# Optimization experiments

Hardware: AMD Instinct MI355X
Metric: run time of the kernel (lower is better)

Reference implementation:

```python
import jax, jax.numpy as jnp
import numpy as np

WINDOW = 128
CAUSAL = True
LOOK_BACKWARD = 1
LOOK_FORWARD = 0  # causal forces look_forward = 0


def _look_around(x, backward, forward, pad_value, dim):
    # pad along window axis (axis=1), then concat shifted slices along `dim`
    nw = x.shape[1]
    pad_cfg = [(0, 0)] * x.ndim
    pad_cfg[1] = (backward, forward)
    padded = jnp.pad(x, pad_cfg, constant_values=pad_value)
    slices = [padded[:, i:i + nw] for i in range(forward + backward + 1)]
    return jnp.concatenate(slices, axis=dim)


def setup_inputs() -> dict:
    key = jax.random.key(0)
    kq, kk, kv = jax.random.split(key, 3)
    shape = (2, 16, 4096, 64)
    return {
        "q": jax.random.normal(kq, shape, dtype=jnp.float32),
        "k": jax.random.normal(kk, shape, dtype=jnp.float32),
        "v": jax.random.normal(kv, shape, dtype=jnp.float32),
    }


def reference(q, k, v):
    b, h, t, e = q.shape
    scale = e ** (-0.5)
    windows = t // WINDOW  # t assumed divisible by WINDOW (pad_to_multiple is no-op)

    # merge batch and heads, bucket into windows
    bq = q.reshape(b * h, windows, WINDOW, e)
    bk = k.reshape(b * h, windows, WINDOW, e)
    bv = v.reshape(b * h, windows, WINDOW, e)

    # look-around gather of key/value windows: j-dim = WINDOW*(1+back+fwd)
    bk = _look_around(bk, LOOK_BACKWARD, LOOK_FORWARD, 0.0, dim=2)
    bv = _look_around(bv, LOOK_BACKWARD, LOOK_FORWARD, 0.0, dim=2)

    # positional indices for masking
    bq_t = jnp.arange(t).reshape(1, windows, WINDOW)
    bq_k = _look_around(bq_t, LOOK_BACKWARD, LOOK_FORWARD, -1, dim=2)

    mask = (bq_k == -1)[:, :, None, :]  # (1, w, 1, j) padded positions
    if CAUSAL:
        mask = mask | (bq_t[:, :, :, None] < bq_k[:, :, None, :])

    dots = jnp.einsum('bwie,bwje->bwij', bq * scale, bk)
    mask_value = -jnp.finfo(dots.dtype).max
    dots = jnp.where(mask, mask_value, dots)
    attn = jax.nn.softmax(dots.astype(jnp.float32), axis=-1).astype(dots.dtype)
    out = jnp.einsum('bwij,bwje->bwie', attn, bv)
    return out.reshape(b, h, t, e)
```

## Files before the change

### kernel.cpp

```cpp
#include <hip/hip_runtime.h>

#define T_DIM 4096
#define E_DIM 64
#define WIN   128
#define NWIN  (T_DIM / WIN)
#define VT_LD 264
#define PS_LD 36

typedef __bf16  bf16x8 __attribute__((ext_vector_type(8)));
typedef __bf16  bf16x4 __attribute__((ext_vector_type(4)));
typedef float   f32x16 __attribute__((ext_vector_type(16)));

__global__ __launch_bounds__(256, 2)
void la_fwd(const float* __restrict__ Q, const float* __restrict__ K,
            const float* __restrict__ V, float* __restrict__ O)
{
  __shared__ __bf16 Vt[E_DIM * VT_LD];
  __shared__ __bf16 Ps[4 * 32 * PS_LD];

  const int tid  = threadIdx.x;
  const int lane = tid & 63;
  const int wid  = tid >> 6;
  const int col  = lane & 31;
  const int half = lane >> 5;

  const int w  = blockIdx.x;
  const int bh = blockIdx.y;

  const float* Qb = Q + (size_t)bh * T_DIM * E_DIM;
  const float* Kb = K + (size_t)bh * T_DIM * E_DIM;
  const float* Vb = V + (size_t)bh * T_DIM * E_DIM;
  float*       Ob = O + (size_t)bh * T_DIM * E_DIM;

  const int q0 = w * WIN;
  const int k0 = (w - 1) * WIN;

  {
    const int j = tid;
    int jg = k0 + j; if (jg < 0) jg = 0;
    const float* vrow = Vb + (size_t)jg * E_DIM;
#pragma unroll
    for (int c4 = 0; c4 < 16; ++c4) {
      const float4 vv = *(const float4*)(vrow + c4 * 4);
      const int e = c4 * 4;
      Vt[(e + 0) * VT_LD + j] = (__bf16)vv.x;
      Vt[(e + 1) * VT_LD + j] = (__bf16)vv.y;
      Vt[(e + 2) * VT_LD + j] = (__bf16)vv.z;
      Vt[(e + 3) * VT_LD + j] = (__bf16)vv.w;
    }
  }

  const float QS = 0.125f * 1.44269504088896340736f;
  bf16x8 aq[4];
  {
    const float* qrow = Qb + (size_t)(q0 + wid * 32 + col) * E_DIM;
#pragma unroll
    for (int c = 0; c < 4; ++c) {
      const float* p = qrow + c * 16 + half * 8;
      const float4 x = *(const float4*)(p);
      const float4 y = *(const float4*)(p + 4);
      bf16x8 a;
      a[0] = (__bf16)(x.x * QS); a[1] = (__bf16)(x.y * QS);
      a[2] = (__bf16)(x.z * QS); a[3] = (__bf16)(x.w * QS);
      a[4] = (__bf16)(y.x * QS); a[5] = (__bf16)(y.y * QS);
      a[6] = (__bf16)(y.z * QS); a[7] = (__bf16)(y.w * QS);
      aq[c] = a;
    }
  }

  __syncthreads();

  f32x16 sacc[8];
#pragma unroll
  for (int kb = 0; kb < 8; ++kb)
#pragma unroll
    for (int r = 0; r < 16; ++r) sacc[kb][r] = 0.0f;

#pragma unroll
  for (int kb = 0; kb < 8; ++kb) {
    int jg = k0 + kb * 32 + col; if (jg < 0) jg = 0;
    const float* krow = Kb + (size_t)jg * E_DIM;
#pragma unroll
    for (int c = 0; c < 4; ++c) {
      const float* p = krow + c * 16 + half * 8;
      const float4 x = *(const float4*)(p);
      const float4 y = *(const float4*)(p + 4);
      bf16x8 b;
      b[0] = (__bf16)x.x; b[1] = (__bf16)x.y; b[2] = (__bf16)x.z; b[3] = (__bf16)x.w;
      b[4] = (__bf16)y.x; b[5] = (__bf16)y.y; b[6] = (__bf16)y.z; b[7] = (__bf16)y.w;
      sacc[kb] = __builtin_amdgcn_mfma_f32_32x32x16_bf16(aq[c], b, sacc[kb], 0, 0, 0);
    }
  }

  float rinv[16];
#pragma unroll
  for (int r = 0; r < 16; ++r) {
    const int row  = (r & 3) + 8 * (r >> 2) + 4 * half;
    const int iloc = wid * 32 + row;
    float m = -3.0e38f;
#pragma unroll
    for (int kb = 0; kb < 8; ++kb) {
      const int jloc = kb * 32 + col;
      const bool masked = (jloc > iloc + WIN) || (w == 0 && jloc < WIN);
      const float s = masked ? -3.0e38f : sacc[kb][r];
      sacc[kb][r] = s;
      m = fmaxf(m, s);
    }
#pragma unroll
    for (int d = 1; d <= 16; d <<= 1) m = fmaxf(m, __shfl_xor(m, d));
    float l = 0.0f;
#pragma unroll
    for (int kb = 0; kb < 8; ++kb) {
      const float p = __builtin_amdgcn_exp2f(sacc[kb][r] - m);
      sacc[kb][r] = p;
      l += p;
    }
#pragma unroll
    for (int d = 1; d <= 16; d <<= 1) l += __shfl_xor(l, d);
    rinv[r] = __builtin_amdgcn_rcpf(l);
  }

  f32x16 oacc[2];
#pragma unroll
  for (int et = 0; et < 2; ++et)
#pragma unroll
    for (int r = 0; r < 16; ++r) oacc[et][r] = 0.0f;

  __bf16* myPs = Ps + wid * (32 * PS_LD);
#pragma unroll
  for (int kb = 0; kb < 8; ++kb) {
#pragma unroll
    for (int r = 0; r < 16; ++r) {
      const int row = (r & 3) + 8 * (r >> 2) + 4 * half;
      myPs[row * PS_LD + col] = (__bf16)sacc[kb][r];
    }
    bf16x8 ap[2];
#pragma unroll
    for (int c2 = 0; c2 < 2; ++c2) {
      const __bf16* rp = myPs + col * PS_LD + c2 * 16 + half * 8;
      union { bf16x8 v8; bf16x4 v4[2]; } u;
      u.v4[0] = *(const bf16x4*)(rp);
      u.v4[1] = *(const bf16x4*)(rp + 4);
      ap[c2] = u.v8;
    }
#pragma unroll
    for (int c2 = 0; c2 < 2; ++c2) {
      const int j0 = kb * 32 + c2 * 16 + half * 8;
#pragma unroll
      for (int et = 0; et < 2; ++et) {
        const int e = et * 32 + col;
        const bf16x8 bv = *(const bf16x8*)(Vt + e * VT_LD + j0);
        oacc[et] = __builtin_amdgcn_mfma_f32_32x32x16_bf16(ap[c2], bv, oacc[et], 0, 0, 0);
      }
    }
  }

#pragma unroll
  for (int r = 0; r < 16; ++r) {
    const int row = (r & 3) + 8 * (r >> 2) + 4 * half;
    const int ig  = q0 + wid * 32 + row;
    float* op = Ob + (size_t)ig * E_DIM;
    op[col]      = oacc[0][r] * rinv[r];
    op[col + 32] = oacc[1][r] * rinv[r];
  }
}

extern "C" void kernel_launch(void* const* d_in, const int* in_sizes, int n_in,
                              void* d_out, int out_size, void* d_ws, size_t ws_size,
                              hipStream_t stream) {
  const float* Q = (const float*)d_in[0];
  const float* K = (const float*)d_in[1];
  const float* V = (const float*)d_in[2];
  float*       O = (float*)d_out;
  const int bh = in_sizes[0] / (T_DIM * E_DIM);
  dim3 grid(NWIN, bh);
  la_fwd<<<grid, 256, 0, stream>>>(Q, K, V, O);
}
```

Before: 160.2 us.

## Stream K/V windows through LDS with online softmax and skip masked tiles

Restructures the kernel into two stages, previous window then current window. Each stage stages K (bf16, row layout) and transposed V into LDS and runs an online-softmax flash-style loop over 32-key blocks. Fully masked blocks (future keys, and the previous window when w==0) are skipped, row reductions use DPP/swizzle instead of shfl, and occupancy is raised to 3 blocks per SM. This removes redundant masked MMA/exp work and the large score register array, at the cost of extra syncs and per-block rescaling.

```diff
diff --git a/kernel.cpp b/kernel.cpp
--- a/kernel.cpp
+++ b/kernel.cpp
@@ -4,19 +4,45 @@
 #define E_DIM 64
 #define WIN   128
 #define NWIN  (T_DIM / WIN)
-#define VT_LD 264
+#define KS_LD 72
+#define VT_LD 136
 #define PS_LD 36
 
 typedef __bf16  bf16x8 __attribute__((ext_vector_type(8)));
 typedef __bf16  bf16x4 __attribute__((ext_vector_type(4)));
 typedef float   f32x16 __attribute__((ext_vector_type(16)));
 
-__global__ __launch_bounds__(256, 2)
+template<int CTRL>
+__device__ __forceinline__ float dppf(float x) {
+  return __int_as_float(__builtin_amdgcn_update_dpp(0, __float_as_int(x), CTRL, 0xf, 0xf, false));
+}
+__device__ __forceinline__ float swz16(float x) {
+  return __int_as_float(__builtin_amdgcn_ds_swizzle(__float_as_int(x), 0x401F));
+}
+__device__ __forceinline__ float rmax32(float x) {
+  x = fmaxf(x, dppf<0xB1>(x));
+  x = fmaxf(x, dppf<0x4E>(x));
+  x = fmaxf(x, dppf<0x141>(x));
+  x = fmaxf(x, dppf<0x140>(x));
+  x = fmaxf(x, swz16(x));
+  return x;
+}
+__device__ __forceinline__ float rsum32(float x) {
+  x += dppf<0xB1>(x);
+  x += dppf<0x4E>(x);
+  x += dppf<0x141>(x);
+  x += dppf<0x140>(x);
+  x += swz16(x);
+  return x;
+}
+
+__global__ __launch_bounds__(256, 3)
 void la_fwd(const float* __restrict__ Q, const float* __restrict__ K,
             const float* __restrict__ V, float* __restrict__ O)
 {
+  __shared__ __bf16 Ks[WIN * KS_LD];
   __shared__ __bf16 Vt[E_DIM * VT_LD];
-  __shared__ __bf16 Ps[4 * 32 * PS_LD];
+  __shared__ __bf16 Psm[4 * 32 * PS_LD];
 
   const int tid  = threadIdx.x;
   const int lane = tid & 63;
@@ -33,22 +59,6 @@
   float*       Ob = O + (size_t)bh * T_DIM * E_DIM;
 
   const int q0 = w * WIN;
-  const int k0 = (w - 1) * WIN;
-
-  {
-    const int j = tid;
-    int jg = k0 + j; if (jg < 0) jg = 0;
-    const float* vrow = Vb + (size_t)jg * E_DIM;
-#pragma unroll
-    for (int c4 = 0; c4 < 16; ++c4) {
-      const float4 vv = *(const float4*)(vrow + c4 * 4);
-      const int e = c4 * 4;
-      Vt[(e + 0) * VT_LD + j] = (__bf16)vv.x;
-      Vt[(e + 1) * VT_LD + j] = (__bf16)vv.y;
-      Vt[(e + 2) * VT_LD + j] = (__bf16)vv.z;
-      Vt[(e + 3) * VT_LD + j] = (__bf16)vv.w;
-    }
-  }
 
   const float QS = 0.125f * 1.44269504088896340736f;
   bf16x8 aq[4];
@@ -60,84 +70,71 @@
       const float4 x = *(const float4*)(p);
       const float4 y = *(const float4*)(p + 4);
       bf16x8 a;
-      a[0] = (__bf16)(x.x * QS); a[1] = (__bf16)(x.y * QS);
-      a[2] = (__bf16)(x.z * QS); a[3] = (__bf16)(x.w * QS);
-      a[4] = (__bf16)(y.x * QS); a[5] = (__bf16)(y.y * QS);
-      a[6] = (__bf16)(y.z * QS); a[7] = (__bf16)(y.w * QS);
+      a[0]=(__bf16)(x.x*QS); a[1]=(__bf16)(x.y*QS); a[2]=(__bf16)(x.z*QS); a[3]=(__bf16)(x.w*QS);
+      a[4]=(__bf16)(y.x*QS); a[5]=(__bf16)(y.y*QS); a[6]=(__bf16)(y.z*QS); a[7]=(__bf16)(y.w*QS);
       aq[c] = a;
     }
   }
 
-  __syncthreads();
-
-  f32x16 sacc[8];
+  float mr[16], lr[16];
+  f32x16 oacc[2];
 #pragma unroll
-  for (int kb = 0; kb < 8; ++kb)
-#pragma unroll
-    for (int r = 0; r < 16; ++r) sacc[kb][r] = 0.0f;
-
-#pragma unroll
-  for (int kb = 0; kb < 8; ++kb) {
-    int jg = k0 + kb * 32 + col; if (jg < 0) jg = 0;
-    const float* krow = Kb + (size_t)jg * E_DIM;
-#pragma unroll
-    for (int c = 0; c < 4; ++c) {
-      const float* p = krow + c * 16 + half * 8;
-      const float4 x = *(const float4*)(p);
-      const float4 y = *(const float4*)(p + 4);
-      bf16x8 b;
-      b[0] = (__bf16)x.x; b[1] = (__bf16)x.y; b[2] = (__bf16)x.z; b[3] = (__bf16)x.w;
-      b[4] = (__bf16)y.x; b[5] = (__bf16)y.y; b[6] = (__bf16)y.z; b[7] = (__bf16)y.w;
-      sacc[kb] = __builtin_amdgcn_mfma_f32_32x32x16_bf16(aq[c], b, sacc[kb], 0, 0, 0);
-    }
-  }
-
-  float rinv[16];
-#pragma unroll
-  for (int r = 0; r < 16; ++r) {
-    const int row  = (r & 3) + 8 * (r >> 2) + 4 * half;
-    const int iloc = wid * 32 + row;
-    float m = -3.0e38f;
-#pragma unroll
-    for (int kb = 0; kb < 8; ++kb) {
-      const int jloc = kb * 32 + col;
-      const bool masked = (jloc > iloc + WIN) || (w == 0 && jloc < WIN);
-      const float s = masked ? -3.0e38f : sacc[kb][r];
-      sacc[kb][r] = s;
-      m = fmaxf(m, s);
-    }
-#pragma unroll
-    for (int d = 1; d <= 16; d <<= 1) m = fmaxf(m, __shfl_xor(m, d));
-    float l = 0.0f;
-#pragma unroll
-    for (int kb = 0; kb < 8; ++kb) {
-      const float p = __builtin_amdgcn_exp2f(sacc[kb][r] - m);
-      sacc[kb][r] = p;
-      l += p;
-    }
-#pragma unroll
-    for (int d = 1; d <= 16; d <<= 1) l += __shfl_xor(l, d);
-    rinv[r] = __builtin_amdgcn_rcpf(l);
-  }
-
-  f32x16 oacc[2];
+  for (int r = 0; r < 16; ++r) { mr[r] = -3.0e38f; lr[r] = 0.0f; }
 #pragma unroll
   for (int et = 0; et < 2; ++et)
 #pragma unroll
     for (int r = 0; r < 16; ++r) oacc[et][r] = 0.0f;
 
-  __bf16* myPs = Ps + wid * (32 * PS_LD);
+  __bf16* Ps = Psm + wid * (32 * PS_LD);
+
+  auto stage = [&](int kr0) {
+    const float* kp = Kb + (size_t)kr0 * E_DIM;
+    const float* vp = Vb + (size_t)kr0 * E_DIM;
 #pragma unroll
-  for (int kb = 0; kb < 8; ++kb) {
+    for (int i = 0; i < 8; ++i) {
+      const int fi    = (i << 10) + (tid << 2);
+      const float4 kv = *(const float4*)(kp + fi);
+      const float4 vv = *(const float4*)(vp + fi);
+      const int row  = fi >> 6;
+      const int cole = fi & 63;
+      bf16x4 k4; k4[0]=(__bf16)kv.x; k4[1]=(__bf16)kv.y; k4[2]=(__bf16)kv.z; k4[3]=(__bf16)kv.w;
+      *(bf16x4*)(&Ks[row * KS_LD + cole]) = k4;
+      Vt[(cole + 0) * VT_LD + row] = (__bf16)vv.x;
+      Vt[(cole + 1) * VT_LD + row] = (__bf16)vv.y;
+      Vt[(cole + 2) * VT_LD + row] = (__bf16)vv.z;
+      Vt[(cole + 3) * VT_LD + row] = (__bf16)vv.w;
+    }
+  };
+
+  auto kb_step = [&](int kb, bool diag) {
+    f32x16 s;
+#pragma unroll
+    for (int r = 0; r < 16; ++r) s[r] = 0.0f;
+#pragma unroll
+    for (int c = 0; c < 4; ++c) {
+      const bf16x8 bk = *(const bf16x8*)(&Ks[(kb * 32 + col) * KS_LD + c * 16 + half * 8]);
+      s = __builtin_amdgcn_mfma_f32_32x32x16_bf16(aq[c], bk, s, 0, 0, 0);
+    }
 #pragma unroll
     for (int r = 0; r < 16; ++r) {
       const int row = (r & 3) + 8 * (r >> 2) + 4 * half;
-      myPs[row * PS_LD + col] = (__bf16)sacc[kb][r];
+      float sv = s[r];
+      if (diag && col > row) sv = -3.0e38f;
+      const float mb    = rmax32(sv);
+      const float mnew  = fmaxf(mr[r], mb);
+      const float alpha = __builtin_amdgcn_exp2f(mr[r] - mnew);
+      const float pv    = __builtin_amdgcn_exp2f(sv - mnew);
+      const float ps    = rsum32(pv);
+      lr[r] = lr[r] * alpha + ps;
+      mr[r] = mnew;
+      oacc[0][r] *= alpha;
+      oacc[1][r] *= alpha;
+      Ps[row * PS_LD + col] = (__bf16)pv;
     }
     bf16x8 ap[2];
 #pragma unroll
     for (int c2 = 0; c2 < 2; ++c2) {
-      const __bf16* rp = myPs + col * PS_LD + c2 * 16 + half * 8;
+      const __bf16* rp = Ps + col * PS_LD + c2 * 16 + half * 8;
       union { bf16x8 v8; bf16x4 v4[2]; } u;
       u.v4[0] = *(const bf16x4*)(rp);
       u.v4[1] = *(const bf16x4*)(rp + 4);
@@ -148,20 +145,31 @@
       const int j0 = kb * 32 + c2 * 16 + half * 8;
 #pragma unroll
       for (int et = 0; et < 2; ++et) {
-        const int e = et * 32 + col;
-        const bf16x8 bv = *(const bf16x8*)(Vt + e * VT_LD + j0);
+        const bf16x8 bv = *(const bf16x8*)(&Vt[(et * 32 + col) * VT_LD + j0]);
         oacc[et] = __builtin_amdgcn_mfma_f32_32x32x16_bf16(ap[c2], bv, oacc[et], 0, 0, 0);
       }
     }
+  };
+
+  if (w > 0) {
+    stage(q0 - WIN);
+    __syncthreads();
+#pragma unroll
+    for (int kb = 0; kb < 4; ++kb) kb_step(kb, false);
+    __syncthreads();
   }
+
+  stage(q0);
+  __syncthreads();
+  for (int kb = 0; kb <= wid; ++kb) kb_step(kb, kb == wid);
 
 #pragma unroll
   for (int r = 0; r < 16; ++r) {
-    const int row = (r & 3) + 8 * (r >> 2) + 4 * half;
-    const int ig  = q0 + wid * 32 + row;
-    float* op = Ob + (size_t)ig * E_DIM;
-    op[col]      = oacc[0][r] * rinv[r];
-    op[col + 32] = oacc[1][r] * rinv[r];
+    const int row  = (r & 3) + 8 * (r >> 2) + 4 * half;
+    const float rinv = __builtin_amdgcn_rcpf(lr[r]);
+    float* op = Ob + (size_t)(q0 + wid * 32 + row) * E_DIM;
+    op[col]      = oacc[0][r] * rinv;
+    op[col + 32] = oacc[1][r] * rinv;
   }
 }
 
```

Result: slower. 198.3 us (+23.8%).
